# Kernel tuning notes

Hardware: AMD Instinct MI355X
Metric: run time of the kernel (lower is better)

Reference implementation:

```python
import jax, jax.numpy as jnp
import numpy as np

EMBED_DIM = 1024
N_HEADS = 16
DK = EMBED_DIM // N_HEADS


def setup_inputs() -> dict:
    key = jax.random.key(0)
    ks = jax.random.split(key, 9)
    s = 1.0 / np.sqrt(EMBED_DIM)
    d = EMBED_DIM
    return {
        "x": jax.random.normal(ks[0], (2, 2048, d), dtype=jnp.float32),
        "Wq": jax.random.uniform(ks[1], (d, d), jnp.float32, -s, s),
        "bq": jax.random.uniform(ks[2], (d,), jnp.float32, -s, s),
        "Wk": jax.random.uniform(ks[3], (d, d), jnp.float32, -s, s),
        "bk": jax.random.uniform(ks[4], (d,), jnp.float32, -s, s),
        "Wv": jax.random.uniform(ks[5], (d, d), jnp.float32, -s, s),
        "bv": jax.random.uniform(ks[6], (d,), jnp.float32, -s, s),
        "Wo": jax.random.uniform(ks[7], (d, d), jnp.float32, -s, s),
        "bo": jax.random.uniform(ks[8], (d,), jnp.float32, -s, s),
    }


def reference(x, Wq, bq, Wk, bk, Wv, bv, Wo, bo):
    B, S, D = x.shape
    H, dk = N_HEADS, DK
    # QKV projections
    q = (x @ Wq + bq).reshape(B, S, H, dk).transpose(0, 2, 1, 3)  # [B,H,S,dk]
    k = (x @ Wk + bk).reshape(B, S, H, dk).transpose(0, 2, 1, 3)
    v = (x @ Wv + bv).reshape(B, S, H, dk).transpose(0, 2, 1, 3)
    # scaled dot-product attention with full score matrix (faithful to source)
    scores = jnp.einsum("bhqd,bhkd->bhqk", q, k) / jnp.sqrt(jnp.float32(dk))
    attn = jax.nn.softmax(scores, axis=-1)
    out = jnp.einsum("bhqk,bhkd->bhqd", attn, v)  # [B,H,S,dk]
    out = out.transpose(0, 2, 1, 3).reshape(B, S, D)
    return out @ Wo + bo
```

## Files before the change

### kernel.cpp

```cpp
#include <hip/hip_runtime.h>

typedef unsigned short u16;
typedef unsigned int u32;
typedef __attribute__((ext_vector_type(8))) short short8;
typedef __attribute__((ext_vector_type(4))) float float4v;
typedef __attribute__((ext_vector_type(4))) unsigned int uint4v;

struct alignas(8) U16x4 { u16 x, y, z, w; };

__device__ __forceinline__ u16 f2b(float f) {
    union { float f; unsigned int u; } v; v.f = f;
    unsigned int r = (v.u >> 16) & 1u;
    v.u += 0x7fffu + r;
    return (u16)(v.u >> 16);
}

__device__ __forceinline__ float b2f(u16 u) {
    union { unsigned int u; float f; } v; v.u = ((u32)u) << 16; return v.f;
}

__device__ __forceinline__ u32 cvt_pk_bf16(float lo, float hi) {
    u32 d;
    asm("v_cvt_pk_bf16_f32 %0, %1, %2" : "=v"(d) : "v"(lo), "v"(hi));
    return d;
}

__device__ __forceinline__ void gld16(const u16* g, u16* l) {
    __builtin_amdgcn_global_load_lds(
        (const __attribute__((address_space(1))) void*)g,
        (__attribute__((address_space(3))) void*)l, 16, 0, 0);
}

__device__ __forceinline__ short8 frag8(const u16* base, int row, int cg) {
    return *(const short8*)(base + row * 64 + ((cg ^ (row & 7)) << 3));
}

__global__ __launch_bounds__(256) void prep_kernel(
    const float* __restrict__ x, const float* __restrict__ W0,
    const float* __restrict__ W1, const float* __restrict__ W2,
    const float* __restrict__ W3, u16* __restrict__ xb,
    u16* __restrict__ T0, u16* __restrict__ T1,
    u16* __restrict__ T2, u16* __restrict__ T3) {
    __shared__ float tile[32][33];
    int id = blockIdx.x;
    if (id < 4096) {
        size_t i = ((size_t)id * 256 + threadIdx.x) * 4;
        float4 v = *(const float4*)(x + i);
        U16x4 o;
        o.x = f2b(v.x); o.y = f2b(v.y); o.z = f2b(v.z); o.w = f2b(v.w);
        *(U16x4*)(xb + i) = o;
        return;
    }
    int r = id - 4096;
    int z = r >> 10, tl = r & 1023;
    const float* W = (z == 0) ? W0 : (z == 1) ? W1 : (z == 2) ? W2 : W3;
    u16* T = (z == 0) ? T0 : (z == 1) ? T1 : (z == 2) ? T2 : T3;
    int t = threadIdx.x;
    int tx = t & 31, ty = t >> 5;
    int bn = (tl & 31) * 32, bk = (tl >> 5) * 32;
#pragma unroll
    for (int p = 0; p < 4; ++p) {
        int k = ty + p * 8;
        tile[k][tx] = W[(size_t)(bk + k) * 1024 + bn + tx];
    }
    __syncthreads();
#pragma unroll
    for (int p = 0; p < 4; ++p) {
        int n = ty + p * 8;
        T[(size_t)(bn + n) * 1024 + bk + tx] = f2b(tile[tx][n]);
    }
}

__global__ __launch_bounds__(256, 3) void qkv_kernel(
    const u16* __restrict__ X, const u16* __restrict__ WT,
    const float* __restrict__ bq, const float* __restrict__ bk, const float* __restrict__ bv,
    u16* __restrict__ Qo, u16* __restrict__ Ko, u16* __restrict__ VTo) {
    __shared__ __align__(16) u16 As[128 * 64];
    __shared__ __align__(16) u16 Bs[128 * 64];
    int id = blockIdx.x;
    int m = (id & 7) | (((id >> 3) & 3) << 3);
    int n = id >> 5;
    int t = threadIdx.x;
    int m0 = m * 128, n0 = n * 128;
    int lane = t & 63, wid = t >> 6;
    int wr = wid >> 1, wc = wid & 1;
    int l16 = lane & 15, quad = lane >> 4;
    int rl = lane >> 3, cs = lane & 7;

    const u16* gsrc = (wid < 2) ? X : WT;
    int gbase = (wid < 2) ? m0 : n0;
    u16* ldst = (wid < 2) ? As : Bs;
    int h8 = wid & 1;

    float4v acc[4][4];
    float4v zero4 = {0.f, 0.f, 0.f, 0.f};
#pragma unroll
    for (int i = 0; i < 4; ++i)
#pragma unroll
        for (int j = 0; j < 4; ++j) acc[i][j] = zero4;

    for (int k0 = 0; k0 < 1024; k0 += 64) {
        __syncthreads();
#pragma unroll
        for (int p = 0; p < 8; ++p) {
            int q = h8 * 8 + p;
            int row = q * 8 + rl;
            int c = cs ^ (row & 7);
            gld16(gsrc + (size_t)(gbase + row) * 1024 + k0 + c * 8, ldst + q * 512);
        }
        __syncthreads();
#pragma unroll
        for (int ks = 0; ks < 64; ks += 32) {
            int cg = (ks >> 3) + quad;
            short8 af[4], bf[4];
#pragma unroll
            for (int i = 0; i < 4; ++i)
                af[i] = frag8(As, wr * 64 + i * 16 + l16, cg);
#pragma unroll
            for (int j = 0; j < 4; ++j)
                bf[j] = frag8(Bs, wc * 64 + j * 16 + l16, cg);
#pragma unroll
            for (int i = 0; i < 4; ++i)
#pragma unroll
                for (int j = 0; j < 4; ++j)
                    acc[i][j] = __builtin_amdgcn_mfma_f32_16x16x32_bf16(
                        af[i], bf[j], acc[i][j], 0, 0, 0);
        }
    }

    int z = n >> 3;
    const float QSCALE = 0.18033688011112042f;
#pragma unroll
    for (int j = 0; j < 4; ++j) {
        int n1 = n0 + wc * 64 + j * 16 + l16;
        int col = n1 & 1023;
        float bcol = (z == 0) ? bq[col] : (z == 1) ? bk[col] : bv[col];
#pragma unroll
        for (int i = 0; i < 4; ++i) {
            int mbase = m0 + wr * 64 + i * 16 + quad * 4;
            if (z == 0) {
#pragma unroll
                for (int r = 0; r < 4; ++r)
                    Qo[(size_t)(mbase + r) * 1024 + col] =
                        f2b((acc[i][j][r] + bcol) * QSCALE);
            } else if (z == 1) {
#pragma unroll
                for (int r = 0; r < 4; ++r)
                    Ko[(size_t)(mbase + r) * 1024 + col] =
                        f2b(acc[i][j][r] + bcol);
            } else {
                int bidx = mbase >> 11, s = mbase & 2047;
                size_t base =
                    ((size_t)((bidx * 16 + (col >> 6)) * 64 + (col & 63))) * 2048 + s;
                U16x4 pk;
                pk.x = f2b(acc[i][j][0] + bcol);
                pk.y = f2b(acc[i][j][1] + bcol);
                pk.z = f2b(acc[i][j][2] + bcol);
                pk.w = f2b(acc[i][j][3] + bcol);
                *(U16x4*)(VTo + base) = pk;
            }
        }
    }
}

__global__ __launch_bounds__(256, 4) void oproj_kernel(const u16* __restrict__ Op,
                                                       const float* __restrict__ lp,
                                                       const u16* __restrict__ WoT,
                                                       const float* __restrict__ bias,
                                                       float* __restrict__ out) {
    __shared__ __align__(16) u16 As[64 * 64];
    __shared__ __align__(16) u16 Bs[2][64 * 64];
    __shared__ float invs[64][16];
    int id = blockIdx.x;
    int m = (id & 7) | (((id >> 3) & 7) << 3);
    int n = id >> 6;
    int t = threadIdx.x;
    int m0 = m * 64, n0 = n * 64;
    int lane = t & 63, wid = t >> 6;
    int l16 = lane & 15, quad = lane >> 4;
    int rl = lane >> 3, cs = lane & 7;

#pragma unroll
    for (int e = t; e < 1024; e += 256) {
        int row = e >> 4, hh = e & 15;
        int qg = (m0 + row) * 16 + hh;
        invs[row][hh] = 1.0f / (lp[qg] + lp[65536 + qg]);
    }

    int row0 = wid * 16 + rl;
    int row1 = row0 + 8;
    size_t g0 = (size_t)(m0 + row0) * 1024 + cs * 8;
    size_t g1 = (size_t)(m0 + row1) * 1024 + cs * 8;

    float4v acc[4];
    float4v zero4 = {0.f, 0.f, 0.f, 0.f};
#pragma unroll
    for (int i = 0; i < 4; ++i) acc[i] = zero4;

#pragma unroll
    for (int p = 0; p < 2; ++p) {
        int blk = wid * 2 + p;
        int row = blk * 8 + rl;
        int c = cs ^ (row & 7);
        gld16(WoT + (size_t)(n0 + row) * 1024 + 0 + c * 8, &Bs[0][blk * 512]);
    }
    short8 oc00 = *(const short8*)(Op + g0);
    short8 oc01 = *(const short8*)(Op + 4194304 + g0);
    short8 oc10 = *(const short8*)(Op + g1);
    short8 oc11 = *(const short8*)(Op + 4194304 + g1);

    for (int k0 = 0; k0 < 1024; k0 += 64) {
        int buf = (k0 >> 6) & 1;
        int hh = k0 >> 6;
        __syncthreads();

        {
            float iv0 = invs[row0][hh], iv1 = invs[row1][hh];
            uint4v w0, w1;
#pragma unroll
            for (int q2 = 0; q2 < 4; ++q2) {
                float a0 = (b2f((u16)oc00[q2 * 2]) + b2f((u16)oc01[q2 * 2])) * iv0;
                float b0 = (b2f((u16)oc00[q2 * 2 + 1]) + b2f((u16)oc01[q2 * 2 + 1])) * iv0;
                w0[q2] = cvt_pk_bf16(a0, b0);
                float a1 = (b2f((u16)oc10[q2 * 2]) + b2f((u16)oc11[q2 * 2])) * iv1;
                float b1 = (b2f((u16)oc10[q2 * 2 + 1]) + b2f((u16)oc11[q2 * 2 + 1])) * iv1;
                w1[q2] = cvt_pk_bf16(a1, b1);
            }
            *(uint4v*)(As + row0 * 64 + ((cs ^ (row0 & 7)) << 3)) = w0;
            *(uint4v*)(As + row1 * 64 + ((cs ^ (row1 & 7)) << 3)) = w1;
        }
        __syncthreads();

        if (k0 + 64 < 1024) {
#pragma unroll
            for (int p = 0; p < 2; ++p) {
                int blk = wid * 2 + p;
                int row = blk * 8 + rl;
                int c = cs ^ (row & 7);
                gld16(WoT + (size_t)(n0 + row) * 1024 + (k0 + 64) + c * 8,
                      &Bs[buf ^ 1][blk * 512]);
            }
            oc00 = *(const short8*)(Op + g0 + k0 + 64);
            oc01 = *(const short8*)(Op + 4194304 + g0 + k0 + 64);
            oc10 = *(const short8*)(Op + g1 + k0 + 64);
            oc11 = *(const short8*)(Op + 4194304 + g1 + k0 + 64);
        }

#pragma unroll
        for (int ks = 0; ks < 64; ks += 32) {
            int cg = (ks >> 3) + quad;
            short8 af[4];
#pragma unroll
            for (int i = 0; i < 4; ++i) af[i] = frag8(As, i * 16 + l16, cg);
            short8 bf = frag8(&Bs[buf][0], wid * 16 + l16, cg);
#pragma unroll
            for (int i = 0; i < 4; ++i)
                acc[i] = __builtin_amdgcn_mfma_f32_16x16x32_bf16(
                    af[i], bf, acc[i], 0, 0, 0);
        }
    }

    int n1 = n0 + wid * 16 + l16;
    float bvl = bias[n1];
#pragma unroll
    for (int i = 0; i < 4; ++i) {
        int mbase = m0 + i * 16 + quad * 4;
#pragma unroll
        for (int r = 0; r < 4; ++r)
            out[(size_t)(mbase + r) * 1024 + n1] = acc[i][r] + bvl;
    }
}

__global__ __launch_bounds__(256, 4) void flash_kernel(const u16* __restrict__ Q,
                                                       const u16* __restrict__ Kn,
                                                       const u16* __restrict__ VT,
                                                       u16* __restrict__ Opart,
                                                       float* __restrict__ lpart) {
    __shared__ __align__(16) u16 Ks[2][64 * 64];
    __shared__ __align__(16) u16 Vs[2][64 * 64];

    int id = blockIdx.x;
    int bh = (id & 7) | (((id >> 3) & 3) << 3);
    int rest = id >> 5;
    int qb = rest & 15, kvz = rest >> 4;
    int b = bh >> 4, h = bh & 15;
    int t = threadIdx.x;
    int wid = t >> 6, lane = t & 63;
    int l16 = lane & 15, quad = lane >> 4;
    int rl = lane >> 3, cs = lane & 7;
    int q0 = qb * 128 + wid * 32;
    size_t kbase = (size_t)(b * 2048) * 1024 + h * 64;
    size_t vbase = (size_t)(bh * 64) * 2048;
    int kv0 = kvz * 1024;

    short8 qf[2][2];
#pragma unroll
    for (int j = 0; j < 2; ++j)
#pragma unroll
        for (int kk = 0; kk < 2; ++kk)
            qf[j][kk] = *(const short8*)(
                Q + ((size_t)(b * 2048 + q0 + j * 16 + l16)) * 1024 + h * 64 +
                kk * 32 + quad * 8);

    float4v oacc[2][4];
    float4v den[2];
    float4v zero4 = {0.f, 0.f, 0.f, 0.f};
    const short8 ones8 = {(short)0x3F80, (short)0x3F80, (short)0x3F80, (short)0x3F80,
                          (short)0x3F80, (short)0x3F80, (short)0x3F80, (short)0x3F80};
#pragma unroll
    for (int ip = 0; ip < 2; ++ip) {
        den[ip] = zero4;
#pragma unroll
        for (int jd = 0; jd < 4; ++jd) oacc[ip][jd] = zero4;
    }

#define STAGE_KV(buf, kv)                                                     \
    {                                                                         \
        _Pragma("unroll") for (int p2 = 0; p2 < 2; ++p2) {                    \
            int p = wid * 2 + p2;                                             \
            int row = p * 8 + rl;                                             \
            int c = cs ^ (row & 7);                                           \
            int key = (((row >> 4) & 1) << 5) | (((row >> 2) & 3) << 3) |     \
                      (((row >> 5) & 1) << 2) | (row & 3);                    \
            gld16(Kn + kbase + (size_t)((kv) + key) * 1024 + c * 8,           \
                  &Ks[buf][p * 512]);                                         \
            gld16(VT + vbase + (size_t)row * 2048 + (kv) + c * 8,             \
                  &Vs[buf][p * 512]);                                         \
        }                                                                     \
    }

    STAGE_KV(0, kv0);

    for (int kvi = 0; kvi < 16; ++kvi) {
        int buf = kvi & 1;
        __syncthreads();
        if (kvi + 1 < 16) STAGE_KV(buf ^ 1, kv0 + (kvi + 1) * 64);

        u32 pw[2][4][2];
#pragma unroll
        for (int i = 0; i < 4; ++i) {
            float4v s0 = zero4, s1 = zero4;
            __builtin_amdgcn_s_setprio(1);
#pragma unroll
            for (int kk = 0; kk < 2; ++kk) {
                short8 kf = frag8(&Ks[buf][0], i * 16 + l16, kk * 4 + quad);
                s0 = __builtin_amdgcn_mfma_f32_16x16x32_bf16(kf, qf[0][kk], s0, 0, 0, 0);
                s1 = __builtin_amdgcn_mfma_f32_16x16x32_bf16(kf, qf[1][kk], s1, 0, 0, 0);
            }
            __builtin_amdgcn_s_setprio(0);
#pragma unroll
            for (int j = 0; j < 2; ++j) {
                float4v s = (j == 0) ? s0 : s1;
                float e0f = __builtin_amdgcn_exp2f(s[0]);
                float e1f = __builtin_amdgcn_exp2f(s[1]);
                float e2f = __builtin_amdgcn_exp2f(s[2]);
                float e3f = __builtin_amdgcn_exp2f(s[3]);
                pw[j][i][0] = cvt_pk_bf16(e0f, e1f);
                pw[j][i][1] = cvt_pk_bf16(e2f, e3f);
            }
        }

        __builtin_amdgcn_s_setprio(1);
#pragma unroll
        for (int kk = 0; kk < 2; ++kk) {
            int cg = kk * 4 + quad;
            short8 vf[4];
#pragma unroll
            for (int jd = 0; jd < 4; ++jd)
                vf[jd] = frag8(&Vs[buf][0], jd * 16 + l16, cg);
#pragma unroll
            for (int j = 0; j < 2; ++j) {
                union { uint4v u; short8 s; } pu;
                pu.u = (uint4v){pw[j][kk][0], pw[j][kk][1],
                                pw[j][2 + kk][0], pw[j][2 + kk][1]};
#pragma unroll
                for (int jd = 0; jd < 4; ++jd)
                    oacc[j][jd] = __builtin_amdgcn_mfma_f32_16x16x32_bf16(
                        pu.s, vf[jd], oacc[j][jd], 0, 0, 0);
                den[j] = __builtin_amdgcn_mfma_f32_16x16x32_bf16(
                    pu.s, ones8, den[j], 0, 0, 0);
            }
        }
        __builtin_amdgcn_s_setprio(0);
    }
#undef STAGE_KV

    size_t obase = (size_t)kvz * 4194304;
#pragma unroll
    for (int ip = 0; ip < 2; ++ip)
#pragma unroll
        for (int r = 0; r < 4; ++r) {
            int q = q0 + ip * 16 + quad * 4 + r;
#pragma unroll
            for (int jd = 0; jd < 4; ++jd)
                Opart[obase + ((size_t)(b * 2048 + q)) * 1024 + h * 64 +
                      jd * 16 + l16] = f2b(oacc[ip][jd][r]);
        }
    if (l16 == 0) {
#pragma unroll
        for (int j = 0; j < 2; ++j)
#pragma unroll
            for (int r = 0; r < 4; ++r) {
                int q = q0 + j * 16 + quad * 4 + r;
                lpart[kvz * 65536 + (b * 2048 + q) * 16 + h] = den[j][r];
            }
    }
}

extern "C" void kernel_launch(void* const* d_in, const int* in_sizes, int n_in,
                              void* d_out, int out_size, void* d_ws, size_t ws_size,
                              hipStream_t stream) {
    const float* x  = (const float*)d_in[0];
    const float* Wq = (const float*)d_in[1];
    const float* bq = (const float*)d_in[2];
    const float* Wk = (const float*)d_in[3];
    const float* bk = (const float*)d_in[4];
    const float* Wv = (const float*)d_in[5];
    const float* bv = (const float*)d_in[6];
    const float* Wo = (const float*)d_in[7];
    const float* bo = (const float*)d_in[8];
    float* out = (float*)d_out;

    char* ws = (char*)d_ws;
    const size_t MB = 1024 * 1024;
    u16* xb  = (u16*)(ws);
    u16* wqt = (u16*)(ws + 8 * MB);
    u16* wkt = (u16*)(ws + 10 * MB);
    u16* wvt = (u16*)(ws + 12 * MB);
    u16* wot = (u16*)(ws + 14 * MB);
    u16* qb_ = (u16*)(ws + 16 * MB);
    u16* kb_ = (u16*)(ws + 24 * MB);
    u16* vt_ = (u16*)(ws + 32 * MB);
    u16* op_ = (u16*)(ws + 48 * MB);
    float* lp_ = (float*)(ws + 64 * MB);

    prep_kernel<<<8192, 256, 0, stream>>>(x, Wq, Wk, Wv, Wo, xb,
                                          wqt, wkt, wvt, wot);
    qkv_kernel<<<768, 256, 0, stream>>>(xb, wqt, bq, bk, bv,
                                        qb_, kb_, vt_);
    flash_kernel<<<1024, 256, 0, stream>>>(qb_, kb_, vt_, op_, lp_);
    oproj_kernel<<<1024, 256, 0, stream>>>(op_, lp_, wot, bo, out);
}
```

Measured before the change: 183.5 us.

## Split K/V prefetch waits in attention; single-buffer the output projection

The attention kernel now issues K and V tile loads as separate groups. It replaces the full __syncthreads with explicit vmcnt waits plus raw barriers, so the QK^T stage starts once K has landed while V is still in flight. A second wait and barrier before the PV stage makes sure V is ready. The output-projection kernel drops its double-buffered WoT tile and register prefetch of the partial outputs: each k-step loads and combines its data directly, which cuts LDS and register use but removes the load/compute overlap there. The hand-counted vmcnt values depend on exact load ordering and are fragile if the code is rescheduled.

```diff
diff --git a/kernel.cpp b/kernel.cpp
--- a/kernel.cpp
+++ b/kernel.cpp
@@ -169,7 +169,7 @@
                                                        const float* __restrict__ bias,
                                                        float* __restrict__ out) {
     __shared__ __align__(16) u16 As[64 * 64];
-    __shared__ __align__(16) u16 Bs[2][64 * 64];
+    __shared__ __align__(16) u16 Bs[64 * 64];
     __shared__ float invs[64][16];
     int id = blockIdx.x;
     int m = (id & 7) | (((id >> 3) & 7) << 3);
@@ -182,77 +182,51 @@
 
 #pragma unroll
     for (int e = t; e < 1024; e += 256) {
-        int row = e >> 4, hh = e & 15;
-        int qg = (m0 + row) * 16 + hh;
-        invs[row][hh] = 1.0f / (lp[qg] + lp[65536 + qg]);
-    }
-
-    int row0 = wid * 16 + rl;
-    int row1 = row0 + 8;
-    size_t g0 = (size_t)(m0 + row0) * 1024 + cs * 8;
-    size_t g1 = (size_t)(m0 + row1) * 1024 + cs * 8;
+        int row = e >> 4, h = e & 15;
+        int qg = (m0 + row) * 16 + h;
+        invs[row][h] = 1.0f / (lp[qg] + lp[65536 + qg]);
+    }
 
     float4v acc[4];
     float4v zero4 = {0.f, 0.f, 0.f, 0.f};
 #pragma unroll
     for (int i = 0; i < 4; ++i) acc[i] = zero4;
 
-#pragma unroll
-    for (int p = 0; p < 2; ++p) {
-        int blk = wid * 2 + p;
-        int row = blk * 8 + rl;
-        int c = cs ^ (row & 7);
-        gld16(WoT + (size_t)(n0 + row) * 1024 + 0 + c * 8, &Bs[0][blk * 512]);
-    }
-    short8 oc00 = *(const short8*)(Op + g0);
-    short8 oc01 = *(const short8*)(Op + 4194304 + g0);
-    short8 oc10 = *(const short8*)(Op + g1);
-    short8 oc11 = *(const short8*)(Op + 4194304 + g1);
-
     for (int k0 = 0; k0 < 1024; k0 += 64) {
-        int buf = (k0 >> 6) & 1;
-        int hh = k0 >> 6;
         __syncthreads();
-
-        {
-            float iv0 = invs[row0][hh], iv1 = invs[row1][hh];
-            uint4v w0, w1;
+#pragma unroll
+        for (int p = 0; p < 2; ++p) {
+            int blk = wid * 2 + p;
+            int row = blk * 8 + rl;
+            int c = cs ^ (row & 7);
+            gld16(WoT + (size_t)(n0 + row) * 1024 + k0 + c * 8, Bs + blk * 512);
+        }
+        int h = k0 >> 6;
+#pragma unroll
+        for (int p = 0; p < 2; ++p) {
+            int blk = wid * 2 + p;
+            int row = blk * 8 + rl;
+            size_t goff = (size_t)(m0 + row) * 1024 + k0 + cs * 8;
+            short8 o0 = *(const short8*)(Op + goff);
+            short8 o1 = *(const short8*)(Op + 4194304 + goff);
+            float iv = invs[row][h];
+            uint4v w;
 #pragma unroll
             for (int q2 = 0; q2 < 4; ++q2) {
-                float a0 = (b2f((u16)oc00[q2 * 2]) + b2f((u16)oc01[q2 * 2])) * iv0;
-                float b0 = (b2f((u16)oc00[q2 * 2 + 1]) + b2f((u16)oc01[q2 * 2 + 1])) * iv0;
-                w0[q2] = cvt_pk_bf16(a0, b0);
-                float a1 = (b2f((u16)oc10[q2 * 2]) + b2f((u16)oc11[q2 * 2])) * iv1;
-                float b1 = (b2f((u16)oc10[q2 * 2 + 1]) + b2f((u16)oc11[q2 * 2 + 1])) * iv1;
-                w1[q2] = cvt_pk_bf16(a1, b1);
-            }
-            *(uint4v*)(As + row0 * 64 + ((cs ^ (row0 & 7)) << 3)) = w0;
-            *(uint4v*)(As + row1 * 64 + ((cs ^ (row1 & 7)) << 3)) = w1;
+                float a = (b2f((u16)o0[q2 * 2]) + b2f((u16)o1[q2 * 2])) * iv;
+                float bb = (b2f((u16)o0[q2 * 2 + 1]) + b2f((u16)o1[q2 * 2 + 1])) * iv;
+                w[q2] = cvt_pk_bf16(a, bb);
+            }
+            *(uint4v*)(As + row * 64 + ((cs ^ (row & 7)) << 3)) = w;
         }
         __syncthreads();
-
-        if (k0 + 64 < 1024) {
-#pragma unroll
-            for (int p = 0; p < 2; ++p) {
-                int blk = wid * 2 + p;
-                int row = blk * 8 + rl;
-                int c = cs ^ (row & 7);
-                gld16(WoT + (size_t)(n0 + row) * 1024 + (k0 + 64) + c * 8,
-                      &Bs[buf ^ 1][blk * 512]);
-            }
-            oc00 = *(const short8*)(Op + g0 + k0 + 64);
-            oc01 = *(const short8*)(Op + 4194304 + g0 + k0 + 64);
-            oc10 = *(const short8*)(Op + g1 + k0 + 64);
-            oc11 = *(const short8*)(Op + 4194304 + g1 + k0 + 64);
-        }
-
 #pragma unroll
         for (int ks = 0; ks < 64; ks += 32) {
             int cg = (ks >> 3) + quad;
             short8 af[4];
 #pragma unroll
             for (int i = 0; i < 4; ++i) af[i] = frag8(As, i * 16 + l16, cg);
-            short8 bf = frag8(&Bs[buf][0], wid * 16 + l16, cg);
+            short8 bf = frag8(Bs, wid * 16 + l16, cg);
 #pragma unroll
             for (int i = 0; i < 4; ++i)
                 acc[i] = __builtin_amdgcn_mfma_f32_16x16x32_bf16(
@@ -314,7 +288,7 @@
         for (int jd = 0; jd < 4; ++jd) oacc[ip][jd] = zero4;
     }
 
-#define STAGE_KV(buf, kv)                                                     \
+#define STAGE_K(buf, kv)                                                      \
     {                                                                         \
         _Pragma("unroll") for (int p2 = 0; p2 < 2; ++p2) {                    \
             int p = wid * 2 + p2;                                             \
@@ -324,17 +298,32 @@
                       (((row >> 5) & 1) << 2) | (row & 3);                    \
             gld16(Kn + kbase + (size_t)((kv) + key) * 1024 + c * 8,           \
                   &Ks[buf][p * 512]);                                         \
+        }                                                                     \
+    }
+#define STAGE_V(buf, kv)                                                      \
+    {                                                                         \
+        _Pragma("unroll") for (int p2 = 0; p2 < 2; ++p2) {                    \
+            int p = wid * 2 + p2;                                             \
+            int row = p * 8 + rl;                                             \
+            int c = cs ^ (row & 7);                                           \
             gld16(VT + vbase + (size_t)row * 2048 + (kv) + c * 8,             \
                   &Vs[buf][p * 512]);                                         \
         }                                                                     \
     }
 
-    STAGE_KV(0, kv0);
+    STAGE_K(0, kv0);
+    STAGE_V(0, kv0);
 
     for (int kvi = 0; kvi < 16; ++kvi) {
         int buf = kvi & 1;
-        __syncthreads();
-        if (kvi + 1 < 16) STAGE_KV(buf ^ 1, kv0 + (kvi + 1) * 64);
+        asm volatile("s_waitcnt vmcnt(2)" ::: "memory");
+        __builtin_amdgcn_s_barrier();
+        __builtin_amdgcn_sched_barrier(0);
+        bool stage = (kvi + 1 < 16);
+        if (stage) {
+            STAGE_K(buf ^ 1, kv0 + (kvi + 1) * 64);
+            STAGE_V(buf ^ 1, kv0 + (kvi + 1) * 64);
+        }
 
         u32 pw[2][4][2];
 #pragma unroll
@@ -360,6 +349,14 @@
             }
         }
 
+        if (stage) {
+            asm volatile("s_waitcnt vmcnt(4)" ::: "memory");
+        } else {
+            asm volatile("s_waitcnt vmcnt(0)" ::: "memory");
+        }
+        __builtin_amdgcn_s_barrier();
+        __builtin_amdgcn_sched_barrier(0);
+
         __builtin_amdgcn_s_setprio(1);
 #pragma unroll
         for (int kk = 0; kk < 2; ++kk) {
@@ -383,7 +380,8 @@
         }
         __builtin_amdgcn_s_setprio(0);
     }
-#undef STAGE_KV
+#undef STAGE_K
+#undef STAGE_V
 
     size_t obase = (size_t)kvz * 4194304;
 #pragma unroll
```

Measured after the change: 186.1 us. About the same (+1.4%).
